# Performance work log

Hardware: AMD Instinct MI355X
Metric: run time of the kernel (lower is better)

Reference implementation:

```python
import jax, jax.numpy as jnp
import numpy as np

IN_MODES = (8, 8, 8, 8)
OUT_MODES = (8, 8, 8, 8)
R = 16
RANKS = (1, R, R, R, 1)
BATCH = 8192
PROD_IN = int(np.prod(IN_MODES))   # 4096
PROD_OUT = int(np.prod(OUT_MODES))  # 4096


def setup_inputs() -> dict:
    key = jax.random.key(0)
    ks = jax.random.split(key, 6)
    # matches reset_normal() init scale
    CONST = ((0.05 ** 2 / np.prod(RANKS)) ** (1.0 / (len(RANKS) - 1))) ** 0.5
    P0 = jax.random.normal(ks[0], (OUT_MODES[0] * IN_MODES[0], R, 1), jnp.float32) * CONST
    P1 = jax.random.normal(ks[1], (OUT_MODES[1] * IN_MODES[1], R, R), jnp.float32) * CONST
    P2 = jax.random.normal(ks[2], (OUT_MODES[2] * IN_MODES[2], R, R), jnp.float32) * CONST
    P3 = jax.random.normal(ks[3], (OUT_MODES[3] * IN_MODES[3], R, 1), jnp.float32) * CONST
    bias = jnp.zeros((PROD_OUT,), jnp.float32)
    x = jax.random.normal(ks[5], (BATCH, PROD_IN), jnp.float32)
    return {"x": x, "P0": P0, "P1": P1, "P2": P2, "P3": P3, "bias": bias}


def _cayley(P):
    # Batched Cayley transform: Q = (I - A) @ inv(I + A), A skew from triu(P,1).
    # P: (n, r, r)
    T = jnp.triu(P, 1)
    A = T - jnp.swapaxes(T, -1, -2)
    I = jnp.eye(P.shape[-1], dtype=P.dtype)
    return jnp.einsum('nij,njk->nik', I - A, jnp.linalg.inv(I + A))


def _core(Q, o, m, r_in, r_out, first):
    # Q: (o*m, r, c) stacked in (j, k) order -> U: (r, o, m, c) as in getU
    r, c = Q.shape[1], Q.shape[2]
    U = Q.reshape(o, m, r, c).transpose(2, 0, 1, 3)  # (r, o, m, c)
    if first:
        U = jnp.swapaxes(U, 0, 3)  # (c=1, o, m, r)
    return U.reshape(o * r_out, m * r_in)  # G_i: (o_i * ranks[i+1], m_i * ranks[i])


def _build_cores(P0, P1, P2, P3):
    G0 = _core(P0, OUT_MODES[0], IN_MODES[0], RANKS[0], RANKS[1], True)
    G1 = _core(_cayley(P1), OUT_MODES[1], IN_MODES[1], RANKS[1], RANKS[2], False)
    G2 = _core(_cayley(P2), OUT_MODES[2], IN_MODES[2], RANKS[2], RANKS[3], False)
    G3 = _core(P3, OUT_MODES[3], IN_MODES[3], RANKS[3], RANKS[4], False)
    return [G0, G1, G2, G3]


def _tt_dot(x, G, bias):
    res = x.reshape(-1, PROD_IN).T  # (prod_in, B)
    for ii in range(4):
        res = res.reshape(RANKS[ii] * IN_MODES[ii], -1)
        res = G[ii] @ res                       # (o_i * r_{i+1}, rest)
        res = res.reshape(OUT_MODES[ii], -1).T  # rotate processed mode to back
    res = res.reshape(-1, PROD_OUT)
    return res + bias


def reference(x, P0, P1, P2, P3, bias):
    G = _build_cores(P0, P1, P2, P3)
    return _tt_dot(x, G, bias)
```

## Files before the change

### kernel.cpp

```cpp
#include <hip/hip_runtime.h>
#include <hip/hip_bf16.h>

typedef __attribute__((ext_vector_type(8))) short sh8;
typedef __attribute__((ext_vector_type(16))) float fx16;
typedef __attribute__((ext_vector_type(4))) unsigned int u32x4;

__device__ __forceinline__ unsigned short f2bits(float a) {
  union { __hip_bfloat16 h; unsigned short u; } c;
  c.h = __float2bfloat16(a);
  return c.u;
}
__device__ __forceinline__ unsigned int pk2(float a, float b) {
  return (unsigned int)f2bits(a) | ((unsigned int)f2bits(b) << 16);
}
__device__ __forceinline__ fx16 fzero16() {
  fx16 z;
  #pragma unroll
  for (int i = 0; i < 16; ++i) z[i] = 0.0f;
  return z;
}

#define SWAP32(a, b) asm volatile("v_permlane32_swap_b32 %0, %1" : "+v"(a), "+v"(b))

__global__ void k_cayley(const float* __restrict__ P1, const float* __restrict__ P2,
                         float* __restrict__ Qout) {
  int t = blockIdx.x * blockDim.x + threadIdx.x;
  int mat = t >> 4;
  int row = t & 15;
  if (mat >= 128) return;
  const float* P = (mat < 64) ? (P1 + mat * 256) : (P2 + (mat - 64) * 256);
  float M[16], Rr[16];
  #pragma unroll
  for (int j = 0; j < 16; ++j) {
    float a = 0.0f;
    if (j > row) a = P[row * 16 + j];
    if (j < row) a = -P[j * 16 + row];
    float d = (j == row) ? 1.0f : 0.0f;
    M[j]  = d + a;
    Rr[j] = d - a;
  }
  int gbase = (threadIdx.x & 63) & ~15;
  #pragma unroll
  for (int k = 0; k < 16; ++k) {
    float pkk = __shfl(M[k], gbase + k);
    float inv = 1.0f / pkk;
    float pM[16], pR[16];
    #pragma unroll
    for (int j = 0; j < 16; ++j) {
      pM[j] = __shfl(M[j], gbase + k) * inv;
      pR[j] = __shfl(Rr[j], gbase + k) * inv;
    }
    if (row == k) {
      #pragma unroll
      for (int j = 0; j < 16; ++j) { M[j] = pM[j]; Rr[j] = pR[j]; }
    } else {
      float f = M[k];
      #pragma unroll
      for (int j = 0; j < 16; ++j) { M[j] -= f * pM[j]; Rr[j] -= f * pR[j]; }
    }
  }
  float* qo = Qout + mat * 256 + row * 16;
  #pragma unroll
  for (int j = 0; j < 16; ++j) qo[j] = Rr[j];
}

__global__ void k_build(const float* __restrict__ P0, const float* __restrict__ P3,
                        const float* __restrict__ Qbuf,
                        unsigned short* __restrict__ W1, unsigned short* __restrict__ W2) {
  int t = blockIdx.x * blockDim.x + threadIdx.x;
  if (t >= 131072) return;
  const float* Q1 = Qbuf;
  const float* Q2 = Qbuf + 16384;
  int e  = t & 65535;
  int r  = e & 7;
  int l  = (e >> 3) & 63;
  int kx = (e >> 9) & 3;
  int mt = (e >> 11) & 1;
  int t2 = (e >> 12) & 15;
  int h8 = ((l >> 5) << 3);
  float acc = 0.0f;
  if (t < 65536) {
    int m = mt * 32 + (l & 31);
    int q = kx * 16 + h8 + r;
    int j0 = m >> 3, j1 = m & 7, i0 = q >> 3, i1 = q & 7;
    #pragma unroll
    for (int t1 = 0; t1 < 16; ++t1) {
      float c0 = P0[(j0 * 8 + (t1 >> 1)) * 16 + ((t1 & 1) * 8 + i0)];
      int a1 = j1 * 16 + t2, u1 = t1 * 8 + i1;
      float c1 = Q1[((a1 & 7) * 8 + (u1 >> 4)) * 256 + (a1 >> 3) * 16 + (u1 & 15)];
      acc += c0 * c1;
    }
    W1[e] = f2bits(acc);
  } else {
    int n = mt * 32 + (l & 31);
    int s = kx * 16 + h8 + r;
    int j2 = n >> 3, j3 = n & 7, i2 = s >> 3, i3 = s & 7;
    #pragma unroll
    for (int t3 = 0; t3 < 16; ++t3) {
      int a2 = j2 * 16 + t3, u2 = t2 * 8 + i2;
      float c2 = Q2[((a2 & 7) * 8 + (u2 >> 4)) * 256 + (a2 >> 3) * 16 + (u2 & 15)];
      float c3 = P3[((t3 & 7) * 8 + i3) * 16 + (j3 * 2 + (t3 >> 3))];
      acc += c2 * c3;
    }
    W2[e] = f2bits(acc);
  }
}

__global__ __launch_bounds__(256, 2) void k_main(
    const float* __restrict__ x,
    const unsigned short* __restrict__ W1,
    const unsigned short* __restrict__ W2,
    const float* __restrict__ bias,
    float* __restrict__ out) {
  __shared__ __align__(16) char XsT[4 * 8192];

  const int tid  = threadIdx.x;
  const int lane = tid & 63;
  const int w    = tid >> 6;
  const int h    = lane >> 5;
  const int l31  = lane & 31;
  const size_t b = (size_t)blockIdx.x * 4 + w;

  char* myX = XsT + w * 8192;
  const float* xb = x + b * 4096;

  {
    const int s = lane;
    const unsigned sw = ((unsigned)(s & 7)) << 4;
    char* base = myX + s * 128;
    #pragma unroll
    for (int c = 0; c < 4; ++c) {
      unsigned int d[8];
      #pragma unroll
      for (int jj = 0; jj < 8; ++jj) {
        float a  = xb[(c * 16 + 2 * jj + 0) * 64 + s];
        float bq = xb[(c * 16 + 2 * jj + 1) * 64 + s];
        d[jj] = pk2(a, bq);
      }
      u32x4 v0 = {d[0], d[1], d[2], d[3]};
      u32x4 v1 = {d[4], d[5], d[6], d[7]};
      *(u32x4*)(base + (((unsigned)(c * 32)) ^ sw))      = v0;
      *(u32x4*)(base + (((unsigned)(c * 32 + 16)) ^ sw)) = v1;
    }
  }
  asm volatile("s_waitcnt lgkmcnt(0)" ::: "memory");
  __builtin_amdgcn_sched_barrier(0);

  sh8 af[2][4];
  #pragma unroll
  for (int st = 0; st < 2; ++st)
    #pragma unroll
    for (int kq = 0; kq < 4; ++kq) {
      int srow = st * 32 + l31;
      unsigned boff = (unsigned)srow * 128 +
                      (((unsigned)(kq * 32 + h * 16)) ^ (((unsigned)(srow & 7)) << 4));
      af[st][kq] = *(const sh8*)(myX + boff);
    }

  fx16 accO[2][2];
  #pragma unroll
  for (int a = 0; a < 2; ++a)
    #pragma unroll
    for (int bq = 0; bq < 2; ++bq) accO[a][bq] = fzero16();

  const sh8* w1f = (const sh8*)W1;
  const sh8* w2f = (const sh8*)W2;

  #pragma unroll 2
  for (int t2 = 0; t2 < 16; ++t2) {
    sh8 b1[2][4];
    #pragma unroll
    for (int mt = 0; mt < 2; ++mt)
      #pragma unroll
      for (int kq = 0; kq < 4; ++kq)
        b1[mt][kq] = w1f[t2 * 512 + (mt * 4 + kq) * 64 + lane];

    fx16 accY[2][2];
    #pragma unroll
    for (int a = 0; a < 2; ++a)
      #pragma unroll
      for (int bq = 0; bq < 2; ++bq) accY[a][bq] = fzero16();

    __builtin_amdgcn_s_setprio(1);
    #pragma unroll
    for (int mt = 0; mt < 2; ++mt)
      #pragma unroll
      for (int kq = 0; kq < 4; ++kq) {
        accY[0][mt] = __builtin_amdgcn_mfma_f32_32x32x16_bf16(af[0][kq], b1[mt][kq], accY[0][mt], 0, 0, 0);
        accY[1][mt] = __builtin_amdgcn_mfma_f32_32x32x16_bf16(af[1][kq], b1[mt][kq], accY[1][mt], 0, 0, 0);
      }
    __builtin_amdgcn_s_setprio(0);

    sh8 ga[2][4];
    #pragma unroll
    for (int st = 0; st < 2; ++st)
      #pragma unroll
      for (int mt = 0; mt < 2; ++mt) {
        fx16 Y = accY[st][mt];
        unsigned int P0 = pk2(Y[0],  Y[1]),  P1 = pk2(Y[2],  Y[3]);
        unsigned int P2 = pk2(Y[4],  Y[5]),  P3 = pk2(Y[6],  Y[7]);
        unsigned int P4 = pk2(Y[8],  Y[9]),  P5 = pk2(Y[10], Y[11]);
        unsigned int P6 = pk2(Y[12], Y[13]), P7 = pk2(Y[14], Y[15]);
        SWAP32(P0, P2); SWAP32(P1, P3);
        SWAP32(P4, P6); SWAP32(P5, P7);
        union { u32x4 u; sh8 s8; } c0, c1;
        c0.u = (u32x4){P0, P1, P2, P3};
        c1.u = (u32x4){P4, P5, P6, P7};
        ga[mt][st * 2 + 0] = c0.s8;
        ga[mt][st * 2 + 1] = c1.s8;
      }

    sh8 b2[2][4];
    #pragma unroll
    for (int nt = 0; nt < 2; ++nt)
      #pragma unroll
      for (int ks = 0; ks < 4; ++ks)
        b2[nt][ks] = w2f[t2 * 512 + (nt * 4 + ks) * 64 + lane];

    __builtin_amdgcn_s_setprio(1);
    #pragma unroll
    for (int nt = 0; nt < 2; ++nt)
      #pragma unroll
      for (int ks = 0; ks < 4; ++ks) {
        accO[0][nt] = __builtin_amdgcn_mfma_f32_32x32x16_bf16(ga[0][ks], b2[nt][ks], accO[0][nt], 0, 0, 0);
        accO[1][nt] = __builtin_amdgcn_mfma_f32_32x32x16_bf16(ga[1][ks], b2[nt][ks], accO[1][nt], 0, 0, 0);
      }
    __builtin_amdgcn_s_setprio(0);
  }

  float* ob = out + b * 4096;
  #pragma unroll
  for (int mt = 0; mt < 2; ++mt)
    #pragma unroll
    for (int nt = 0; nt < 2; ++nt) {
      #pragma unroll
      for (int reg = 0; reg < 16; ++reg) {
        int m = mt * 32 + (reg & 3) + 8 * (reg >> 2) + 4 * h;
        int n = nt * 32 + l31;
        int o = m * 64 + n;
        ob[o] = accO[mt][nt][reg] + bias[o];
      }
    }
}

extern "C" void kernel_launch(void* const* d_in, const int* in_sizes, int n_in,
                              void* d_out, int out_size, void* d_ws, size_t ws_size,
                              hipStream_t stream) {
  (void)n_in; (void)out_size; (void)ws_size;
  const float* x    = (const float*)d_in[0];
  const float* P0   = (const float*)d_in[1];
  const float* P1   = (const float*)d_in[2];
  const float* P2   = (const float*)d_in[3];
  const float* P3   = (const float*)d_in[4];
  const float* bias = (const float*)d_in[5];
  float* out = (float*)d_out;

  float* Qbuf = (float*)d_ws;
  unsigned short* W1 = (unsigned short*)((char*)d_ws + 131072);
  unsigned short* W2 = (unsigned short*)((char*)d_ws + 262144);

  k_cayley<<<8, 256, 0, stream>>>(P1, P2, Qbuf);
  k_build<<<512, 256, 0, stream>>>(P0, P3, Qbuf, W1, W2);

  int batch = in_sizes[0] / 4096;
  k_main<<<batch / 4, 256, 0, stream>>>(x, W1, W2, bias, out);
}
```

Measured before the change: 168.1 us.

## Split each batch element across two waves by output half to raise occupancy

Each batch element is now handled by two waves, each computing one half of the intermediate m-dimension (mh) and its share of the output, instead of one wave doing the whole element. This halves per-wave accumulators and register pressure, allowing launch bounds of 3 blocks per CU and twice as many blocks. The x tile is loaded cooperatively with a block-wide barrier, and waves stagger their t2 start index so concurrent waves read different W1/W2 slices. Each wave still recomputes the full first-stage contraction rows for its half, and the W2 fragments are loaded inline right before each MFMA, which may expose load latency.

After: 186.8 us. 1.11x slower.

```diff
diff --git a/kernel.cpp b/kernel.cpp
--- a/kernel.cpp
+++ b/kernel.cpp
@@ -106,46 +106,49 @@
   }
 }
 
-__global__ __launch_bounds__(256, 2) void k_main(
+__global__ __launch_bounds__(256, 3) void k_main(
     const float* __restrict__ x,
     const unsigned short* __restrict__ W1,
     const unsigned short* __restrict__ W2,
     const float* __restrict__ bias,
     float* __restrict__ out) {
-  __shared__ __align__(16) char XsT[4 * 8192];
+  __shared__ __align__(16) char XsT[2 * 8192];
 
   const int tid  = threadIdx.x;
   const int lane = tid & 63;
   const int w    = tid >> 6;
   const int h    = lane >> 5;
   const int l31  = lane & 31;
-  const size_t b = (size_t)blockIdx.x * 4 + w;
-
-  char* myX = XsT + w * 8192;
-  const float* xb = x + b * 4096;
+  const int elem = w >> 1;
+  const int mh   = w & 1;
+  const size_t b = (size_t)blockIdx.x * 2 + elem;
 
   {
-    const int s = lane;
+    int e  = tid >> 7;
+    int s  = tid & 63;
+    int qh = (tid >> 6) & 1;
+    const float* xb = x + ((size_t)blockIdx.x * 2 + e) * 4096;
     const unsigned sw = ((unsigned)(s & 7)) << 4;
-    char* base = myX + s * 128;
-    #pragma unroll
-    for (int c = 0; c < 4; ++c) {
+    char* base = XsT + e * 8192 + s * 128;
+    #pragma unroll
+    for (int c = 0; c < 2; ++c) {
+      int qb = qh * 32 + c * 16;
       unsigned int d[8];
       #pragma unroll
       for (int jj = 0; jj < 8; ++jj) {
-        float a  = xb[(c * 16 + 2 * jj + 0) * 64 + s];
-        float bq = xb[(c * 16 + 2 * jj + 1) * 64 + s];
+        float a  = xb[(qb + 2 * jj + 0) * 64 + s];
+        float bq = xb[(qb + 2 * jj + 1) * 64 + s];
         d[jj] = pk2(a, bq);
       }
       u32x4 v0 = {d[0], d[1], d[2], d[3]};
       u32x4 v1 = {d[4], d[5], d[6], d[7]};
-      *(u32x4*)(base + (((unsigned)(c * 32)) ^ sw))      = v0;
-      *(u32x4*)(base + (((unsigned)(c * 32 + 16)) ^ sw)) = v1;
-    }
-  }
-  asm volatile("s_waitcnt lgkmcnt(0)" ::: "memory");
-  __builtin_amdgcn_sched_barrier(0);
-
+      *(u32x4*)(base + (((unsigned)(qb * 2)) ^ sw))      = v0;
+      *(u32x4*)(base + (((unsigned)(qb * 2 + 16)) ^ sw)) = v1;
+    }
+  }
+  __syncthreads();
+
+  const char* myX = XsT + elem * 8192;
   sh8 af[2][4];
   #pragma unroll
   for (int st = 0; st < 2; ++st)
@@ -157,90 +160,73 @@
       af[st][kq] = *(const sh8*)(myX + boff);
     }
 
-  fx16 accO[2][2];
-  #pragma unroll
-  for (int a = 0; a < 2; ++a)
-    #pragma unroll
-    for (int bq = 0; bq < 2; ++bq) accO[a][bq] = fzero16();
+  const fx16 zc = fzero16();
+  fx16 accO[2];
+  accO[0] = zc; accO[1] = zc;
 
   const sh8* w1f = (const sh8*)W1;
   const sh8* w2f = (const sh8*)W2;
 
   #pragma unroll 2
-  for (int t2 = 0; t2 < 16; ++t2) {
-    sh8 b1[2][4];
-    #pragma unroll
-    for (int mt = 0; mt < 2; ++mt)
-      #pragma unroll
-      for (int kq = 0; kq < 4; ++kq)
-        b1[mt][kq] = w1f[t2 * 512 + (mt * 4 + kq) * 64 + lane];
-
-    fx16 accY[2][2];
-    #pragma unroll
-    for (int a = 0; a < 2; ++a)
-      #pragma unroll
-      for (int bq = 0; bq < 2; ++bq) accY[a][bq] = fzero16();
-
+  for (int it = 0; it < 16; ++it) {
+    const int t2 = (it + w * 4) & 15;
+
+    sh8 b1[4];
+    #pragma unroll
+    for (int kq = 0; kq < 4; ++kq)
+      b1[kq] = w1f[t2 * 512 + (mh * 4 + kq) * 64 + lane];
+
+    fx16 accY[2];
     __builtin_amdgcn_s_setprio(1);
     #pragma unroll
-    for (int mt = 0; mt < 2; ++mt)
-      #pragma unroll
-      for (int kq = 0; kq < 4; ++kq) {
-        accY[0][mt] = __builtin_amdgcn_mfma_f32_32x32x16_bf16(af[0][kq], b1[mt][kq], accY[0][mt], 0, 0, 0);
-        accY[1][mt] = __builtin_amdgcn_mfma_f32_32x32x16_bf16(af[1][kq], b1[mt][kq], accY[1][mt], 0, 0, 0);
+    for (int st = 0; st < 2; ++st) {
+      accY[st] = __builtin_amdgcn_mfma_f32_32x32x16_bf16(af[st][0], b1[0], zc, 0, 0, 0);
+      #pragma unroll
+      for (int kq = 1; kq < 4; ++kq)
+        accY[st] = __builtin_amdgcn_mfma_f32_32x32x16_bf16(af[st][kq], b1[kq], accY[st], 0, 0, 0);
+    }
+    __builtin_amdgcn_s_setprio(0);
+
+    sh8 ga[4];
+    #pragma unroll
+    for (int st = 0; st < 2; ++st) {
+      fx16 Y = accY[st];
+      unsigned int P0 = pk2(Y[0],  Y[1]),  P1 = pk2(Y[2],  Y[3]);
+      unsigned int P2 = pk2(Y[4],  Y[5]),  P3 = pk2(Y[6],  Y[7]);
+      unsigned int P4 = pk2(Y[8],  Y[9]),  P5 = pk2(Y[10], Y[11]);
+      unsigned int P6 = pk2(Y[12], Y[13]), P7 = pk2(Y[14], Y[15]);
+      SWAP32(P0, P2); SWAP32(P1, P3);
+      SWAP32(P4, P6); SWAP32(P5, P7);
+      union { u32x4 u; sh8 s8; } c0, c1;
+      c0.u = (u32x4){P0, P1, P2, P3};
+      c1.u = (u32x4){P4, P5, P6, P7};
+      ga[st * 2 + 0] = c0.s8;
+      ga[st * 2 + 1] = c1.s8;
+    }
+
+    __builtin_amdgcn_s_setprio(1);
+    #pragma unroll
+    for (int nt = 0; nt < 2; ++nt) {
+      #pragma unroll
+      for (int ks = 0; ks < 4; ++ks) {
+        sh8 b2 = w2f[t2 * 512 + (nt * 4 + ks) * 64 + lane];
+        accO[nt] = __builtin_amdgcn_mfma_f32_32x32x16_bf16(ga[ks], b2, accO[nt], 0, 0, 0);
       }
+    }
     __builtin_amdgcn_s_setprio(0);
-
-    sh8 ga[2][4];
-    #pragma unroll
-    for (int st = 0; st < 2; ++st)
-      #pragma unroll
-      for (int mt = 0; mt < 2; ++mt) {
-        fx16 Y = accY[st][mt];
-        unsigned int P0 = pk2(Y[0],  Y[1]),  P1 = pk2(Y[2],  Y[3]);
-        unsigned int P2 = pk2(Y[4],  Y[5]),  P3 = pk2(Y[6],  Y[7]);
-        unsigned int P4 = pk2(Y[8],  Y[9]),  P5 = pk2(Y[10], Y[11]);
-        unsigned int P6 = pk2(Y[12], Y[13]), P7 = pk2(Y[14], Y[15]);
-        SWAP32(P0, P2); SWAP32(P1, P3);
-        SWAP32(P4, P6); SWAP32(P5, P7);
-        union { u32x4 u; sh8 s8; } c0, c1;
-        c0.u = (u32x4){P0, P1, P2, P3};
-        c1.u = (u32x4){P4, P5, P6, P7};
-        ga[mt][st * 2 + 0] = c0.s8;
-        ga[mt][st * 2 + 1] = c1.s8;
-      }
-
-    sh8 b2[2][4];
-    #pragma unroll
-    for (int nt = 0; nt < 2; ++nt)
-      #pragma unroll
-      for (int ks = 0; ks < 4; ++ks)
-        b2[nt][ks] = w2f[t2 * 512 + (nt * 4 + ks) * 64 + lane];
-
-    __builtin_amdgcn_s_setprio(1);
-    #pragma unroll
-    for (int nt = 0; nt < 2; ++nt)
-      #pragma unroll
-      for (int ks = 0; ks < 4; ++ks) {
-        accO[0][nt] = __builtin_amdgcn_mfma_f32_32x32x16_bf16(ga[0][ks], b2[nt][ks], accO[0][nt], 0, 0, 0);
-        accO[1][nt] = __builtin_amdgcn_mfma_f32_32x32x16_bf16(ga[1][ks], b2[nt][ks], accO[1][nt], 0, 0, 0);
-      }
-    __builtin_amdgcn_s_setprio(0);
   }
 
   float* ob = out + b * 4096;
   #pragma unroll
-  for (int mt = 0; mt < 2; ++mt)
-    #pragma unroll
-    for (int nt = 0; nt < 2; ++nt) {
-      #pragma unroll
-      for (int reg = 0; reg < 16; ++reg) {
-        int m = mt * 32 + (reg & 3) + 8 * (reg >> 2) + 4 * h;
-        int n = nt * 32 + l31;
-        int o = m * 64 + n;
-        ob[o] = accO[mt][nt][reg] + bias[o];
-      }
-    }
+  for (int nt = 0; nt < 2; ++nt) {
+    #pragma unroll
+    for (int reg = 0; reg < 16; ++reg) {
+      int m = mh * 32 + (reg & 3) + 8 * (reg >> 2) + 4 * h;
+      int n = nt * 32 + l31;
+      int o = m * 64 + n;
+      ob[o] = accO[nt][reg] + bias[o];
+    }
+  }
 }
 
 extern "C" void kernel_launch(void* const* d_in, const int* in_sizes, int n_in,
@@ -263,5 +249,5 @@
   k_build<<<512, 256, 0, stream>>>(P0, P3, Qbuf, W1, W2);
 
   int batch = in_sizes[0] / 4096;
-  k_main<<<batch / 4, 256, 0, stream>>>(x, W1, W2, bias, out);
-}
+  k_main<<<batch / 2, 256, 0, stream>>>(x, W1, W2, bias, out);
+}
```

## Split each sample's m-tiles across wave pairs sharing staged inputs via LDS

Applied to the files above, without the earlier changes.

Each wave now handles one m-half for two batch samples, where before it handled both m-halves of a single sample. Waves read the X tiles staged by their partner wave through shared memory behind a block barrier. Each wave therefore loads only half of W1 per iteration and interleaves two independent sample chains, giving the scheduler more overlap between MFMA and conversion work. The cost is a __syncthreads, twice the LDS reads per wave for the A fragments, and removal of the unroll-2 hint.

Result: faster. 160.5 us (-4.5%).

```diff
diff --git a/kernel.cpp b/kernel.cpp
--- a/kernel.cpp
+++ b/kernel.cpp
@@ -119,15 +119,15 @@
   const int w    = tid >> 6;
   const int h    = lane >> 5;
   const int l31  = lane & 31;
-  const size_t b = (size_t)blockIdx.x * 4 + w;
-
-  char* myX = XsT + w * 8192;
-  const float* xb = x + b * 4096;
+  const int ep   = (w >> 1) * 2;
+  const int mh   = w & 1;
+  const size_t bbase = (size_t)blockIdx.x * 4;
 
   {
     const int s = lane;
+    const float* xb = x + (bbase + w) * 4096;
     const unsigned sw = ((unsigned)(s & 7)) << 4;
-    char* base = myX + s * 128;
+    char* base = XsT + w * 8192 + s * 128;
     #pragma unroll
     for (int c = 0; c < 4; ++c) {
       unsigned int d[8];
@@ -143,73 +143,36 @@
       *(u32x4*)(base + (((unsigned)(c * 32 + 16)) ^ sw)) = v1;
     }
   }
-  asm volatile("s_waitcnt lgkmcnt(0)" ::: "memory");
-  __builtin_amdgcn_sched_barrier(0);
-
-  sh8 af[2][4];
-  #pragma unroll
-  for (int st = 0; st < 2; ++st)
-    #pragma unroll
-    for (int kq = 0; kq < 4; ++kq) {
-      int srow = st * 32 + l31;
-      unsigned boff = (unsigned)srow * 128 +
-                      (((unsigned)(kq * 32 + h * 16)) ^ (((unsigned)(srow & 7)) << 4));
-      af[st][kq] = *(const sh8*)(myX + boff);
-    }
-
+  __syncthreads();
+
+  sh8 af[2][2][4];
+  #pragma unroll
+  for (int e = 0; e < 2; ++e) {
+    const char* myX = XsT + (ep + e) * 8192;
+    #pragma unroll
+    for (int st = 0; st < 2; ++st)
+      #pragma unroll
+      for (int kq = 0; kq < 4; ++kq) {
+        int srow = st * 32 + l31;
+        unsigned boff = (unsigned)srow * 128 +
+                        (((unsigned)(kq * 32 + h * 16)) ^ (((unsigned)(srow & 7)) << 4));
+        af[e][st][kq] = *(const sh8*)(myX + boff);
+      }
+  }
+
+  const fx16 zc = fzero16();
   fx16 accO[2][2];
-  #pragma unroll
-  for (int a = 0; a < 2; ++a)
-    #pragma unroll
-    for (int bq = 0; bq < 2; ++bq) accO[a][bq] = fzero16();
+  accO[0][0] = zc; accO[0][1] = zc;
+  accO[1][0] = zc; accO[1][1] = zc;
 
   const sh8* w1f = (const sh8*)W1;
   const sh8* w2f = (const sh8*)W2;
 
-  #pragma unroll 2
   for (int t2 = 0; t2 < 16; ++t2) {
-    sh8 b1[2][4];
-    #pragma unroll
-    for (int mt = 0; mt < 2; ++mt)
-      #pragma unroll
-      for (int kq = 0; kq < 4; ++kq)
-        b1[mt][kq] = w1f[t2 * 512 + (mt * 4 + kq) * 64 + lane];
-
-    fx16 accY[2][2];
-    #pragma unroll
-    for (int a = 0; a < 2; ++a)
-      #pragma unroll
-      for (int bq = 0; bq < 2; ++bq) accY[a][bq] = fzero16();
-
-    __builtin_amdgcn_s_setprio(1);
-    #pragma unroll
-    for (int mt = 0; mt < 2; ++mt)
-      #pragma unroll
-      for (int kq = 0; kq < 4; ++kq) {
-        accY[0][mt] = __builtin_amdgcn_mfma_f32_32x32x16_bf16(af[0][kq], b1[mt][kq], accY[0][mt], 0, 0, 0);
-        accY[1][mt] = __builtin_amdgcn_mfma_f32_32x32x16_bf16(af[1][kq], b1[mt][kq], accY[1][mt], 0, 0, 0);
-      }
-    __builtin_amdgcn_s_setprio(0);
-
-    sh8 ga[2][4];
-    #pragma unroll
-    for (int st = 0; st < 2; ++st)
-      #pragma unroll
-      for (int mt = 0; mt < 2; ++mt) {
-        fx16 Y = accY[st][mt];
-        unsigned int P0 = pk2(Y[0],  Y[1]),  P1 = pk2(Y[2],  Y[3]);
-        unsigned int P2 = pk2(Y[4],  Y[5]),  P3 = pk2(Y[6],  Y[7]);
-        unsigned int P4 = pk2(Y[8],  Y[9]),  P5 = pk2(Y[10], Y[11]);
-        unsigned int P6 = pk2(Y[12], Y[13]), P7 = pk2(Y[14], Y[15]);
-        SWAP32(P0, P2); SWAP32(P1, P3);
-        SWAP32(P4, P6); SWAP32(P5, P7);
-        union { u32x4 u; sh8 s8; } c0, c1;
-        c0.u = (u32x4){P0, P1, P2, P3};
-        c1.u = (u32x4){P4, P5, P6, P7};
-        ga[mt][st * 2 + 0] = c0.s8;
-        ga[mt][st * 2 + 1] = c1.s8;
-      }
-
+    sh8 b1[4];
+    #pragma unroll
+    for (int kq = 0; kq < 4; ++kq)
+      b1[kq] = w1f[t2 * 512 + (mh * 4 + kq) * 64 + lane];
     sh8 b2[2][4];
     #pragma unroll
     for (int nt = 0; nt < 2; ++nt)
@@ -217,30 +180,91 @@
       for (int ks = 0; ks < 4; ++ks)
         b2[nt][ks] = w2f[t2 * 512 + (nt * 4 + ks) * 64 + lane];
 
+    fx16 accY[2];
     __builtin_amdgcn_s_setprio(1);
     #pragma unroll
+    for (int st = 0; st < 2; ++st) {
+      accY[st] = __builtin_amdgcn_mfma_f32_32x32x16_bf16(af[0][st][0], b1[0], zc, 0, 0, 0);
+      #pragma unroll
+      for (int kq = 1; kq < 4; ++kq)
+        accY[st] = __builtin_amdgcn_mfma_f32_32x32x16_bf16(af[0][st][kq], b1[kq], accY[st], 0, 0, 0);
+    }
+    __builtin_amdgcn_s_setprio(0);
+
+    sh8 ga0[4];
+    #pragma unroll
+    for (int st = 0; st < 2; ++st) {
+      fx16 Y = accY[st];
+      unsigned int P0 = pk2(Y[0],  Y[1]),  P1 = pk2(Y[2],  Y[3]);
+      unsigned int P2 = pk2(Y[4],  Y[5]),  P3 = pk2(Y[6],  Y[7]);
+      unsigned int P4 = pk2(Y[8],  Y[9]),  P5 = pk2(Y[10], Y[11]);
+      unsigned int P6 = pk2(Y[12], Y[13]), P7 = pk2(Y[14], Y[15]);
+      SWAP32(P0, P2); SWAP32(P1, P3);
+      SWAP32(P4, P6); SWAP32(P5, P7);
+      union { u32x4 u; sh8 s8; } c0, c1;
+      c0.u = (u32x4){P0, P1, P2, P3};
+      c1.u = (u32x4){P4, P5, P6, P7};
+      ga0[st * 2 + 0] = c0.s8;
+      ga0[st * 2 + 1] = c1.s8;
+    }
+
+    fx16 accZ[2];
+    __builtin_amdgcn_s_setprio(1);
+    #pragma unroll
+    for (int st = 0; st < 2; ++st) {
+      accZ[st] = __builtin_amdgcn_mfma_f32_32x32x16_bf16(af[1][st][0], b1[0], zc, 0, 0, 0);
+      #pragma unroll
+      for (int kq = 1; kq < 4; ++kq)
+        accZ[st] = __builtin_amdgcn_mfma_f32_32x32x16_bf16(af[1][st][kq], b1[kq], accZ[st], 0, 0, 0);
+    }
+
+    #pragma unroll
     for (int nt = 0; nt < 2; ++nt)
       #pragma unroll
-      for (int ks = 0; ks < 4; ++ks) {
-        accO[0][nt] = __builtin_amdgcn_mfma_f32_32x32x16_bf16(ga[0][ks], b2[nt][ks], accO[0][nt], 0, 0, 0);
-        accO[1][nt] = __builtin_amdgcn_mfma_f32_32x32x16_bf16(ga[1][ks], b2[nt][ks], accO[1][nt], 0, 0, 0);
-      }
+      for (int ks = 0; ks < 4; ++ks)
+        accO[0][nt] = __builtin_amdgcn_mfma_f32_32x32x16_bf16(ga0[ks], b2[nt][ks], accO[0][nt], 0, 0, 0);
     __builtin_amdgcn_s_setprio(0);
-  }
-
-  float* ob = out + b * 4096;
-  #pragma unroll
-  for (int mt = 0; mt < 2; ++mt)
+
+    sh8 ga1[4];
+    #pragma unroll
+    for (int st = 0; st < 2; ++st) {
+      fx16 Y = accZ[st];
+      unsigned int P0 = pk2(Y[0],  Y[1]),  P1 = pk2(Y[2],  Y[3]);
+      unsigned int P2 = pk2(Y[4],  Y[5]),  P3 = pk2(Y[6],  Y[7]);
+      unsigned int P4 = pk2(Y[8],  Y[9]),  P5 = pk2(Y[10], Y[11]);
+      unsigned int P6 = pk2(Y[12], Y[13]), P7 = pk2(Y[14], Y[15]);
+      SWAP32(P0, P2); SWAP32(P1, P3);
+      SWAP32(P4, P6); SWAP32(P5, P7);
+      union { u32x4 u; sh8 s8; } c0, c1;
+      c0.u = (u32x4){P0, P1, P2, P3};
+      c1.u = (u32x4){P4, P5, P6, P7};
+      ga1[st * 2 + 0] = c0.s8;
+      ga1[st * 2 + 1] = c1.s8;
+    }
+
+    __builtin_amdgcn_s_setprio(1);
+    #pragma unroll
+    for (int nt = 0; nt < 2; ++nt)
+      #pragma unroll
+      for (int ks = 0; ks < 4; ++ks)
+        accO[1][nt] = __builtin_amdgcn_mfma_f32_32x32x16_bf16(ga1[ks], b2[nt][ks], accO[1][nt], 0, 0, 0);
+    __builtin_amdgcn_s_setprio(0);
+  }
+
+  #pragma unroll
+  for (int e = 0; e < 2; ++e) {
+    float* ob = out + (bbase + ep + e) * 4096;
     #pragma unroll
     for (int nt = 0; nt < 2; ++nt) {
       #pragma unroll
       for (int reg = 0; reg < 16; ++reg) {
-        int m = mt * 32 + (reg & 3) + 8 * (reg >> 2) + 4 * h;
+        int m = mh * 32 + (reg & 3) + 8 * (reg >> 2) + 4 * h;
         int n = nt * 32 + l31;
         int o = m * 64 + n;
-        ob[o] = accO[mt][nt][reg] + bias[o];
+        ob[o] = accO[e][nt][reg] + bias[o];
       }
     }
+  }
 }
 
 extern "C" void kernel_launch(void* const* d_in, const int* in_sizes, int n_in,
```
